# Kernel tuning notes

Hardware: AMD Instinct MI355X
Metric: run time of the kernel (lower is better)

The kernel has to match this reference:

```python
import jax, jax.numpy as jnp
import numpy as np
import math

D = 2048
NH = 16       # query heads
NKV = 4       # kv heads (GQA)
HD = 128
SOFTCLAMP = 50.0
ROPE_BASE = 10000.0
B = 4
SQ_VLM = 1024
SQ_ACT = 64
S_CACHE = 256


def _heads(x, n):
    # [B,S,n*HD] -> [B,n,S,HD]
    b, s, _ = x.shape
    return x.reshape(b, s, n, HD).transpose(0, 2, 1, 3)


def _rope_cos_sin(pos):
    # pos: [B,S] int -> cos,sin [B,1,S,HD]
    inv_freq = 1.0 / (ROPE_BASE ** (jnp.arange(0, HD, 2, dtype=jnp.float32) / HD))
    freqs = pos.astype(jnp.float32)[..., None] * inv_freq  # [B,S,HD/2]
    emb = jnp.concatenate([freqs, freqs], axis=-1)         # [B,S,HD]
    return jnp.cos(emb)[:, None], jnp.sin(emb)[:, None]


def _apply_rope(x, cos, sin):
    # x: [B,H,S,HD]
    x1, x2 = x[..., : HD // 2], x[..., HD // 2 :]
    rot = jnp.concatenate([-x2, x1], axis=-1)
    return x * cos + rot * sin


def setup_inputs() -> dict:
    key = jax.random.key(0)
    ks = jax.random.split(key, 16)
    sc = lambda d: 1.0 / math.sqrt(d)
    inp = {
        'attention_mask': jnp.zeros((B, 1, SQ_VLM + SQ_ACT, S_CACHE + SQ_VLM + SQ_ACT), jnp.float32),
        'pos_vlm': jnp.broadcast_to(jnp.arange(S_CACHE, S_CACHE + SQ_VLM, dtype=jnp.int32), (B, SQ_VLM)),
        'pos_action': jnp.broadcast_to(jnp.arange(S_CACHE + SQ_VLM, S_CACHE + SQ_VLM + SQ_ACT, dtype=jnp.int32), (B, SQ_ACT)),
        'h_vlm': jax.random.normal(ks[0], (B, SQ_VLM, D), jnp.float32),
        'h_action': jax.random.normal(ks[1], (B, SQ_ACT, D), jnp.float32),
        'k_cache': jax.random.normal(ks[2], (B, NKV, S_CACHE, HD), jnp.float32),
        'v_cache': jax.random.normal(ks[3], (B, NKV, S_CACHE, HD), jnp.float32),
        'Wq_vlm': jax.random.normal(ks[4], (D, NH * HD), jnp.float32) * sc(D),
        'Wk_vlm': jax.random.normal(ks[5], (D, NKV * HD), jnp.float32) * sc(D),
        'Wv_vlm': jax.random.normal(ks[6], (D, NKV * HD), jnp.float32) * sc(D),
        'Wq_act': jax.random.normal(ks[7], (D, NH * HD), jnp.float32) * sc(D),
        'Wk_act': jax.random.normal(ks[8], (D, NKV * HD), jnp.float32) * sc(D),
        'Wv_act': jax.random.normal(ks[9], (D, NKV * HD), jnp.float32) * sc(D),
        'Wo_act': jax.random.normal(ks[10], (NH * HD, D), jnp.float32) * sc(NH * HD),
    }
    return inp


def reference(attention_mask, pos_vlm, pos_action, h_vlm, h_action, k_cache, v_cache,
              Wq_vlm, Wk_vlm, Wv_vlm, Wq_act, Wk_act, Wv_act, Wo_act):
    group = NH // NKV

    def qkv(h, pos, Wq, Wk, Wv):
        q = _heads(h @ Wq, NH)
        k = _heads(h @ Wk, NKV)
        v = _heads(h @ Wv, NKV)
        cos, sin = _rope_cos_sin(pos)
        return _apply_rope(q, cos, sin), _apply_rope(k, cos, sin), v

    q_v, k_v, v_v = qkv(h_vlm, pos_vlm, Wq_vlm, Wk_vlm, Wv_vlm)
    q_a, k_a, v_a = qkv(h_action, pos_action, Wq_act, Wk_act, Wv_act)

    # repeat_kv (GQA) on every KV source, cached mixture first (append_non_active order)
    rep = lambda t: jnp.repeat(t, group, axis=1)  # [B,NKV,S,HD] -> [B,NH,S,HD]
    k = jnp.concatenate([rep(k_cache), rep(k_v), rep(k_a)], axis=2)
    v = jnp.concatenate([rep(v_cache), rep(v_v), rep(v_a)], axis=2)
    q = jnp.concatenate([q_v, q_a], axis=2)  # [B,NH,Sq,HD]

    scores = jnp.einsum('bhqd,bhkd->bhqk', q, k) / math.sqrt(HD)
    scores = jnp.tanh(scores / SOFTCLAMP) * SOFTCLAMP + attention_mask
    w = jax.nn.softmax(scores.astype(jnp.float32), axis=-1).astype(q.dtype)
    out = jnp.einsum('bhqk,bhkd->bhqd', w, v)
    out = out.transpose(0, 2, 1, 3).reshape(B, SQ_VLM + SQ_ACT, NH * HD)

    # split by q_lens; 'vlm' is in post_attn_skip_names -> no o_proj, dropped
    out_action = out[:, SQ_VLM:, :]
    return out_action @ Wo_act
```

## Files before the change

### kernel.cpp

```cpp
#include <hip/hip_runtime.h>
#include <cmath>

#define NH 16
#define NKV 4
#define HD 128
#define DMODEL 2048
#define BB 4
#define SQV 1024
#define SQA 64
#define SCACHE 256
#define STOT 1344
#define SQTOT 1088
#define NSPLIT 7

typedef unsigned short u16;
typedef __attribute__((ext_vector_type(8))) short short8;
typedef __attribute__((ext_vector_type(4))) float f32x4;

__device__ __forceinline__ float b2f(u16 u) {
    union { float f; unsigned int i; } x; x.i = ((unsigned int)u) << 16; return x.f;
}
__device__ __forceinline__ u16 f2b(float f) {
    unsigned int x = __float_as_uint(f);
    x = x + 0x7fffu + ((x >> 16) & 1u);
    return (u16)(x >> 16);
}

__global__ void k_prep(const float* __restrict__ mask,
                       const float* __restrict__ kc, const float* __restrict__ vc,
                       const float* __restrict__ hv, const float* __restrict__ ha,
                       float* __restrict__ cosT, float* __restrict__ sinT,
                       u16* __restrict__ maskS, u16* __restrict__ K_all, u16* __restrict__ V_all,
                       u16* __restrict__ hv16, u16* __restrict__ ha16) {
    int bx = blockIdx.x, tid = threadIdx.x;
    if (bx < 336) {
        int i = bx * 256 + tid;
        if (i < STOT * 64) {
            int p = i >> 6, j = i & 63;
            float inv = __expf(-(float)j * (9.210340371976184f / 64.0f));
            float ang = (float)p * inv;
            cosT[i] = cosf(ang);
            sinT[i] = sinf(ang);
        }
    } else if (bx < 1680) {
        int i = (bx - 336) * 256 + tid;
        int b = i / (SQA * STOT);
        int r = i % (SQA * STOT);
        size_t s = (size_t)b * SQTOT * STOT + (size_t)SQV * STOT + r;
        maskS[i] = f2b(mask[s]);
    } else if (bx < 1936) {
        int i = (bx - 1680) * 256 + tid;
        int e = i * 8;
        int bk = e / (SCACHE * HD);
        int off = e % (SCACHE * HD);
        size_t dst = (size_t)bk * STOT * HD + off;
        const float* fk = kc + e;
        const float* fv = vc + e;
        u16 tk[8], tv[8];
#pragma unroll
        for (int j = 0; j < 8; j++) { tk[j] = f2b(fk[j]); tv[j] = f2b(fv[j]); }
        *(short8*)(K_all + dst) = *(short8*)tk;
        *(short8*)(V_all + dst) = *(short8*)tv;
    } else if (bx < 6032) {
        int i = (bx - 1936) * 256 + tid;
        int e = i * 8;
        const float* f = hv + e;
        float4 a = *(const float4*)f, b = *(const float4*)(f + 4);
        u16 t[8] = {f2b(a.x), f2b(a.y), f2b(a.z), f2b(a.w),
                    f2b(b.x), f2b(b.y), f2b(b.z), f2b(b.w)};
        *(short8*)(hv16 + e) = *(short8*)t;
    } else {
        int i = (bx - 6032) * 256 + tid;
        int e = i * 8;
        const float* f = ha + e;
        float4 a = *(const float4*)f, b = *(const float4*)(f + 4);
        u16 t[8] = {f2b(a.x), f2b(a.y), f2b(a.z), f2b(a.w),
                    f2b(b.x), f2b(b.y), f2b(b.z), f2b(b.w)};
        *(short8*)(ha16 + e) = *(short8*)t;
    }
}

__device__ __forceinline__ void transpose_body(const float* in, u16* out, int N,
                                               int bx, int by) {
    __shared__ __align__(16) u16 t[64 * 66];
    int n0 = bx * 64, k0 = by * 64;
    int tid = threadIdx.x;
    int r = tid >> 3;
    int c8 = (tid & 7) * 8;
#pragma unroll
    for (int h = 0; h < 2; h++) {
        int k = r + h * 32;
        const float* f = in + (size_t)(k0 + k) * N + n0 + c8;
        float4 a = *(const float4*)f, b = *(const float4*)(f + 4);
        u16 vv[8] = {f2b(a.x), f2b(a.y), f2b(a.z), f2b(a.w),
                     f2b(b.x), f2b(b.y), f2b(b.z), f2b(b.w)};
#pragma unroll
        for (int j = 0; j < 8; j++) t[(c8 + j) * 66 + k] = vv[j];
    }
    __syncthreads();
#pragma unroll
    for (int h = 0; h < 2; h++) {
        int n = r + h * 32;
        short8 v;
#pragma unroll
        for (int j = 0; j < 8; j++) ((u16*)&v)[j] = t[n * 66 + c8 + j];
        *(short8*)(out + (size_t)(n0 + n) * 2048 + k0 + c8) = v;
    }
}

__global__ void k_transpose6(const float* w0, u16* o0, const float* w1, u16* o1,
                             const float* w2, u16* o2, const float* w3, u16* o3,
                             const float* w4, u16* o4, const float* w5, u16* o5) {
    int gx = blockIdx.x;
    if (gx < 256)        transpose_body(w0, o0, 512,  gx & 7,  gx >> 3);
    else if (gx < 512)   { int g = gx - 256;  transpose_body(w1, o1, 512,  g & 7,  g >> 3); }
    else if (gx < 768)   { int g = gx - 512;  transpose_body(w2, o2, 512,  g & 7,  g >> 3); }
    else if (gx < 1024)  { int g = gx - 768;  transpose_body(w3, o3, 512,  g & 7,  g >> 3); }
    else if (gx < 2048)  { int g = gx - 1024; transpose_body(w4, o4, 2048, g & 31, g >> 5); }
    else                 { int g = gx - 2048; transpose_body(w5, o5, 2048, g & 31, g >> 5); }
}

__global__ __launch_bounds__(256) void k_gemm_qkv(
    const u16* __restrict__ Avlm, const u16* __restrict__ Aact,
    const u16* __restrict__ WkvT, const u16* __restrict__ WvvT,
    const u16* __restrict__ WqaT, const u16* __restrict__ WkaT, const u16* __restrict__ WvaT,
    const int* __restrict__ pos_vlm, const int* __restrict__ pos_act,
    const float* __restrict__ cosT, const float* __restrict__ sinT,
    u16* __restrict__ Qbuf, u16* __restrict__ K_all, u16* __restrict__ V_all) {
    __shared__ __align__(16) u16 smem[64 * 72 + 128 * 72];
    u16* As = smem;
    u16* Bs = smem + 64 * 72;
    int tid = threadIdx.x;
    int w = tid >> 6, lane = tid & 63;
    int la = lane & 15, lg = lane >> 4;
    int wm = (w & 1) * 32;
    int c2 = w >> 1;
    int ntab[4] = {c2 * 2, c2 * 2 + 1, c2 * 2 + 4, c2 * 2 + 5};
    int vrow = tid >> 3, vcol = (tid & 7) * 8;

    const u16* A; const u16* Bt; int m0, n0;
    int path;
    int kv_or_head = 0;
    if (blockIdx.y < 8) {
        int by = blockIdx.y;
        m0 = blockIdx.x * 64;
        A = Avlm;
        path = (by < 4) ? 0 : 1;
        kv_or_head = by & 3;
        n0 = kv_or_head * 128;
        Bt = (path == 0) ? WkvT : WvvT;
    } else {
        int g = (blockIdx.y - 8) * 64 + blockIdx.x;
        if (g >= 96) return;
        m0 = (g & 3) * 64;
        int ny = g >> 2;
        A = Aact;
        if (ny < 16)      { path = 2; kv_or_head = ny;      Bt = WqaT; n0 = ny * 128; }
        else if (ny < 20) { path = 3; kv_or_head = ny - 16; Bt = WkaT; n0 = (ny - 16) * 128; }
        else              { path = 4; kv_or_head = ny - 20; Bt = WvaT; n0 = (ny - 20) * 128; }
    }

    f32x4 acc[2][4];
#pragma unroll
    for (int i = 0; i < 2; i++)
#pragma unroll
        for (int j = 0; j < 4; j++) acc[i][j] = (f32x4){0.f, 0.f, 0.f, 0.f};

    short8 pa[2], pb[4];
#pragma unroll
    for (int h = 0; h < 2; h++)
        pa[h] = *(const short8*)(A + (size_t)(m0 + vrow + h * 32) * DMODEL + vcol);
#pragma unroll
    for (int h = 0; h < 4; h++)
        pb[h] = *(const short8*)(Bt + (size_t)(n0 + vrow + h * 32) * DMODEL + vcol);

    for (int kb = 0; kb < DMODEL; kb += 64) {
#pragma unroll
        for (int h = 0; h < 2; h++)
            *(short8*)&As[(vrow + h * 32) * 72 + vcol] = pa[h];
#pragma unroll
        for (int h = 0; h < 4; h++)
            *(short8*)&Bs[(vrow + h * 32) * 72 + vcol] = pb[h];
        __syncthreads();
        int kn = (kb + 64 < DMODEL) ? kb + 64 : kb;
#pragma unroll
        for (int h = 0; h < 2; h++)
            pa[h] = *(const short8*)(A + (size_t)(m0 + vrow + h * 32) * DMODEL + kn + vcol);
#pragma unroll
        for (int h = 0; h < 4; h++)
            pb[h] = *(const short8*)(Bt + (size_t)(n0 + vrow + h * 32) * DMODEL + kn + vcol);
#pragma unroll
        for (int kk = 0; kk < 2; kk++) {
            short8 af[2], bf[4];
#pragma unroll
            for (int mt = 0; mt < 2; mt++) af[mt] = *(const short8*)&As[(wm + mt * 16 + la) * 72 + kk * 32 + lg * 8];
#pragma unroll
            for (int nt = 0; nt < 4; nt++) bf[nt] = *(const short8*)&Bs[(ntab[nt] * 16 + la) * 72 + kk * 32 + lg * 8];
#pragma unroll
            for (int mt = 0; mt < 2; mt++)
#pragma unroll
                for (int nt = 0; nt < 4; nt++)
                    acc[mt][nt] = __builtin_amdgcn_mfma_f32_16x16x32_bf16(af[mt], bf[nt], acc[mt][nt], 0, 0, 0);
        }
        __syncthreads();
    }

#pragma unroll
    for (int mt = 0; mt < 2; mt++) {
#pragma unroll
        for (int r = 0; r < 4; r++) {
            int gm = m0 + wm + mt * 16 + lg * 4 + r;
            if (path <= 1) {
                int b = gm >> 10, s = gm & 1023;
                size_t base = ((size_t)(b * NKV + kv_or_head) * STOT + SCACHE + s) * HD;
                if (path == 0) {
                    int pos = pos_vlm[gm];
#pragma unroll
                    for (int i = 0; i < 2; i++) {
                        int dlo = ntab[i] * 16 + la;
                        float x1 = acc[mt][i][r], x2 = acc[mt][i + 2][r];
                        float cs = cosT[pos * 64 + dlo], sn = sinT[pos * 64 + dlo];
                        K_all[base + dlo]      = f2b(x1 * cs - x2 * sn);
                        K_all[base + dlo + 64] = f2b(x2 * cs + x1 * sn);
                    }
                } else {
#pragma unroll
                    for (int i = 0; i < 4; i++) V_all[base + ntab[i] * 16 + la] = f2b(acc[mt][i][r]);
                }
            } else {
                int b = gm >> 6, s = gm & 63;
                if (path == 2) {
                    int pos = pos_act[gm];
                    size_t qb = ((size_t)(b * NH + kv_or_head) * SQA + s) * HD;
#pragma unroll
                    for (int i = 0; i < 2; i++) {
                        int dlo = ntab[i] * 16 + la;
                        float x1 = acc[mt][i][r], x2 = acc[mt][i + 2][r];
                        float cs = cosT[pos * 64 + dlo], sn = sinT[pos * 64 + dlo];
                        Qbuf[qb + dlo]      = f2b(x1 * cs - x2 * sn);
                        Qbuf[qb + dlo + 64] = f2b(x2 * cs + x1 * sn);
                    }
                } else if (path == 3) {
                    int pos = pos_act[gm];
                    size_t base = ((size_t)(b * NKV + kv_or_head) * STOT + SCACHE + SQV + s) * HD;
#pragma unroll
                    for (int i = 0; i < 2; i++) {
                        int dlo = ntab[i] * 16 + la;
                        float x1 = acc[mt][i][r], x2 = acc[mt][i + 2][r];
                        float cs = cosT[pos * 64 + dlo], sn = sinT[pos * 64 + dlo];
                        K_all[base + dlo]      = f2b(x1 * cs - x2 * sn);
                        K_all[base + dlo + 64] = f2b(x2 * cs + x1 * sn);
                    }
                } else {
                    size_t base = ((size_t)(b * NKV + kv_or_head) * STOT + SCACHE + SQV + s) * HD;
#pragma unroll
                    for (int i = 0; i < 4; i++) V_all[base + ntab[i] * 16 + la] = f2b(acc[mt][i][r]);
                }
            }
        }
    }
}

__global__ __launch_bounds__(256) void k_attn_split(
    const u16* __restrict__ Qbuf, const u16* __restrict__ K_all, const u16* __restrict__ V_all,
    const u16* __restrict__ maskS, u16* __restrict__ po, float* __restrict__ pml) {
    int h = blockIdx.x, b = blockIdx.y, p = blockIdx.z;
    int bh = b * NH + h;
    int kvh = h >> 2;
    const u16* Kb = K_all + (size_t)(b * NKV + kvh) * STOT * HD;
    const u16* Vb = V_all + (size_t)(b * NKV + kvh) * STOT * HD;
    const u16* Qb = Qbuf + (size_t)bh * SQA * HD;
    int tid = threadIdx.x, w = tid >> 6, lane = tid & 63;
    int la = lane & 15, lg = lane >> 4;
    __shared__ __align__(16) u16 Ks[64 * 136];
    __shared__ __align__(16) u16 Vs[64 * 130];
    __shared__ __align__(16) u16 Ps[4][16 * 72];
    short8 qf[4];
#pragma unroll
    for (int kk = 0; kk < 4; kk++)
        qf[kk] = *(const short8*)(Qb + (size_t)(w * 16 + la) * HD + kk * 32 + lg * 8);
    f32x4 o_acc[8];
#pragma unroll
    for (int nt = 0; nt < 8; nt++) o_acc[nt] = (f32x4){0.f, 0.f, 0.f, 0.f};
    float m_run[4], l_run[4];
#pragma unroll
    for (int r = 0; r < 4; r++) { m_run[r] = -3e38f; l_run[r] = 0.f; }
    int vr = tid >> 4;
    int vc = (tid & 15) * 8;
    const float scl = 0.08838834764831845f;
    for (int c = 0; c < 3; c++) {
        int g = p * 3 + c;
#pragma unroll
        for (int hh = 0; hh < 4; hh++) {
            int key = vr + hh * 16;
            *(short8*)&Ks[key * 136 + vc] = *(const short8*)(Kb + (size_t)(g * 64 + key) * HD + vc);
            short8 vv = *(const short8*)(Vb + (size_t)(g * 64 + key) * HD + vc);
            unsigned int* d32 = (unsigned int*)&Vs[key * 130 + vc];
#pragma unroll
            for (int q2 = 0; q2 < 4; q2++) d32[q2] = ((unsigned int*)&vv)[q2];
        }
        __syncthreads();
        f32x4 s_acc[4];
#pragma unroll
        for (int nt = 0; nt < 4; nt++) s_acc[nt] = (f32x4){0.f, 0.f, 0.f, 0.f};
#pragma unroll
        for (int kk = 0; kk < 4; kk++) {
#pragma unroll
            for (int nt = 0; nt < 4; nt++) {
                short8 kf = *(const short8*)&Ks[(nt * 16 + la) * 136 + kk * 32 + lg * 8];
                s_acc[nt] = __builtin_amdgcn_mfma_f32_16x16x32_bf16(qf[kk], kf, s_acc[nt], 0, 0, 0);
            }
        }
        float sc[4][4];
#pragma unroll
        for (int nt = 0; nt < 4; nt++) {
            int key = g * 64 + nt * 16 + la;
#pragma unroll
            for (int r = 0; r < 4; r++) {
                int sq = w * 16 + lg * 4 + r;
                float sv = s_acc[nt][r] * scl;
                sv = tanhf(sv * 0.02f) * 50.0f;
                sv += b2f(maskS[((size_t)(b * SQA + sq)) * STOT + key]);
                sc[nt][r] = sv;
            }
        }
#pragma unroll
        for (int r = 0; r < 4; r++) {
            float mx = fmaxf(fmaxf(sc[0][r], sc[1][r]), fmaxf(sc[2][r], sc[3][r]));
#pragma unroll
            for (int sh = 1; sh < 16; sh <<= 1) mx = fmaxf(mx, __shfl_xor(mx, sh, 64));
            float mn = fmaxf(m_run[r], mx);
            float alpha = __expf(m_run[r] - mn);
            m_run[r] = mn;
            float rowsum = 0.f;
#pragma unroll
            for (int nt = 0; nt < 4; nt++) {
                float pv = __expf(sc[nt][r] - mn);
                Ps[w][(lg * 4 + r) * 72 + nt * 16 + la] = f2b(pv);
                rowsum += pv;
            }
#pragma unroll
            for (int sh = 1; sh < 16; sh <<= 1) rowsum += __shfl_xor(rowsum, sh, 64);
            l_run[r] = l_run[r] * alpha + rowsum;
#pragma unroll
            for (int nt = 0; nt < 8; nt++) o_acc[nt][r] *= alpha;
        }
        __syncthreads();
#pragma unroll
        for (int kk = 0; kk < 2; kk++) {
            short8 pf = *(const short8*)&Ps[w][la * 72 + kk * 32 + lg * 8];
#pragma unroll
            for (int nt = 0; nt < 8; nt++) {
                short8 vf;
#pragma unroll
                for (int j = 0; j < 8; j++) ((u16*)&vf)[j] = Vs[(kk * 32 + lg * 8 + j) * 130 + nt * 16 + la];
                o_acc[nt] = __builtin_amdgcn_mfma_f32_16x16x32_bf16(pf, vf, o_acc[nt], 0, 0, 0);
            }
        }
        __syncthreads();
    }
#pragma unroll
    for (int nt = 0; nt < 8; nt++) {
#pragma unroll
        for (int r = 0; r < 4; r++) {
            int sq = w * 16 + lg * 4 + r;
            po[(((size_t)p * 64 + bh) * 64 + sq) * 128 + nt * 16 + la] = f2b(o_acc[nt][r]);
        }
    }
    if (la == 0) {
#pragma unroll
        for (int r = 0; r < 4; r++) {
            int sq = w * 16 + lg * 4 + r;
            size_t mlb = (((size_t)p * 64 + bh) * 64 + sq) * 2;
            pml[mlb] = m_run[r];
            pml[mlb + 1] = l_run[r];
        }
    }
}

__global__ __launch_bounds__(256) void k_attn_red(
    const u16* __restrict__ po, const float* __restrict__ pml, u16* __restrict__ AO) {
    int h = blockIdx.x, b = blockIdx.y;
    int bh = b * NH + h;
    __shared__ float wgt[NSPLIT][64];
    int tid = threadIdx.x;
    if (tid < 64) {
        int q = tid;
        float m[NSPLIT], l[NSPLIT], M = -3e38f;
#pragma unroll
        for (int p = 0; p < NSPLIT; p++) {
            size_t mlb = (((size_t)p * 64 + bh) * 64 + q) * 2;
            m[p] = pml[mlb]; l[p] = pml[mlb + 1];
            M = fmaxf(M, m[p]);
        }
        float L = 0.f;
#pragma unroll
        for (int p = 0; p < NSPLIT; p++) L += l[p] * __expf(m[p] - M);
        float inv = 1.0f / L;
#pragma unroll
        for (int p = 0; p < NSPLIT; p++) wgt[p][q] = __expf(m[p] - M) * inv;
    }
    __syncthreads();
    for (int e = tid; e < 64 * 128; e += 256) {
        int q = e >> 7, d = e & 127;
        float s = 0.f;
#pragma unroll
        for (int p = 0; p < NSPLIT; p++)
            s += b2f(po[(((size_t)p * 64 + bh) * 64 + q) * 128 + d]) * wgt[p][q];
        AO[((size_t)(b * SQA + q)) * 2048 + h * HD + d] = f2b(s);
    }
}

__global__ __launch_bounds__(256) void k_gemm_out(
    const u16* __restrict__ A, const u16* __restrict__ WoT, float* __restrict__ out) {
    __shared__ __align__(16) u16 As[64 * 72];
    __shared__ __align__(16) u16 Bs[64 * 72];
    int m0 = blockIdx.x * 64, n0 = blockIdx.y * 64;
    int tid = threadIdx.x;
    int w = tid >> 6, lane = tid & 63;
    int la = lane & 15, lg = lane >> 4;
    int wm = (w & 1) * 32, wn = (w >> 1) * 32;
    f32x4 acc[2][2];
#pragma unroll
    for (int i = 0; i < 2; i++)
#pragma unroll
        for (int j = 0; j < 2; j++) acc[i][j] = (f32x4){0.f, 0.f, 0.f, 0.f};
    int vrow = tid >> 3, vcol = (tid & 7) * 8;
    short8 pa[2], pb[2];
#pragma unroll
    for (int h = 0; h < 2; h++) {
        pa[h] = *(const short8*)(A   + (size_t)(m0 + vrow + h * 32) * DMODEL + vcol);
        pb[h] = *(const short8*)(WoT + (size_t)(n0 + vrow + h * 32) * DMODEL + vcol);
    }
    for (int kb = 0; kb < DMODEL; kb += 64) {
#pragma unroll
        for (int h = 0; h < 2; h++) {
            *(short8*)&As[(vrow + h * 32) * 72 + vcol] = pa[h];
            *(short8*)&Bs[(vrow + h * 32) * 72 + vcol] = pb[h];
        }
        __syncthreads();
        int kn = (kb + 64 < DMODEL) ? kb + 64 : kb;
#pragma unroll
        for (int h = 0; h < 2; h++) {
            pa[h] = *(const short8*)(A   + (size_t)(m0 + vrow + h * 32) * DMODEL + kn + vcol);
            pb[h] = *(const short8*)(WoT + (size_t)(n0 + vrow + h * 32) * DMODEL + kn + vcol);
        }
#pragma unroll
        for (int kk = 0; kk < 2; kk++) {
            short8 af[2], bf[2];
#pragma unroll
            for (int mt = 0; mt < 2; mt++) af[mt] = *(const short8*)&As[(wm + mt * 16 + la) * 72 + kk * 32 + lg * 8];
#pragma unroll
            for (int nt = 0; nt < 2; nt++) bf[nt] = *(const short8*)&Bs[(wn + nt * 16 + la) * 72 + kk * 32 + lg * 8];
#pragma unroll
            for (int mt = 0; mt < 2; mt++)
#pragma unroll
                for (int nt = 0; nt < 2; nt++)
                    acc[mt][nt] = __builtin_amdgcn_mfma_f32_16x16x32_bf16(af[mt], bf[nt], acc[mt][nt], 0, 0, 0);
        }
        __syncthreads();
    }
#pragma unroll
    for (int mt = 0; mt < 2; mt++) {
#pragma unroll
        for (int r = 0; r < 4; r++) {
            int gm = m0 + wm + mt * 16 + lg * 4 + r;
#pragma unroll
            for (int nt = 0; nt < 2; nt++)
                out[(size_t)gm * DMODEL + n0 + wn + nt * 16 + la] = acc[mt][nt][r];
        }
    }
}

extern "C" void kernel_launch(void* const* d_in, const int* in_sizes, int n_in,
                              void* d_out, int out_size, void* d_ws, size_t ws_size,
                              hipStream_t stream) {
    (void)in_sizes; (void)n_in; (void)out_size;
    const float* mask    = (const float*)d_in[0];
    const int*   pos_vlm = (const int*)d_in[1];
    const int*   pos_act = (const int*)d_in[2];
    const float* h_vlm   = (const float*)d_in[3];
    const float* h_act   = (const float*)d_in[4];
    const float* k_cache = (const float*)d_in[5];
    const float* v_cache = (const float*)d_in[6];
    const float* Wk_vlm  = (const float*)d_in[8];
    const float* Wv_vlm  = (const float*)d_in[9];
    const float* Wq_act  = (const float*)d_in[10];
    const float* Wk_act  = (const float*)d_in[11];
    const float* Wv_act  = (const float*)d_in[12];
    const float* Wo_act  = (const float*)d_in[13];

    const size_t NEED = 65273856;
    if (ws_size < NEED) return;
    char* ws = (char*)d_ws;
    float* cosT  = (float*)(ws + 0);
    float* sinT  = (float*)(ws + 344064);
    u16* K_all   = (u16*)(ws + 688128);
    u16* V_all   = (u16*)(ws + 6193152);
    u16* Qbuf    = (u16*)(ws + 11698176);
    u16* AO      = (u16*)(ws + 12746752);
    u16* WkvT    = (u16*)(ws + 13795328);
    u16* WvvT    = (u16*)(ws + 15892480);
    u16* WqaT    = (u16*)(ws + 17989632);
    u16* WkaT    = (u16*)(ws + 26378240);
    u16* WvaT    = (u16*)(ws + 28475392);
    u16* WoT     = (u16*)(ws + 30572544);
    u16* po      = (u16*)(ws + 38961152);
    float* pml   = (float*)(ws + 46301184);
    u16* maskS   = (u16*)(ws + 46759936);
    u16* hv16    = (u16*)(ws + 47448064);
    u16* ha16    = (u16*)(ws + 64225280);

    hipLaunchKernelGGL(k_prep, dim3(6288), dim3(256), 0, stream,
                       mask, k_cache, v_cache, h_vlm, h_act,
                       cosT, sinT, maskS, K_all, V_all, hv16, ha16);
    hipLaunchKernelGGL(k_transpose6, dim3(3072), dim3(256), 0, stream,
                       Wk_vlm, WkvT, Wv_vlm, WvvT, Wk_act, WkaT, Wv_act, WvaT,
                       Wq_act, WqaT, Wo_act, WoT);
    hipLaunchKernelGGL(k_gemm_qkv, dim3(64, 10), dim3(256), 0, stream,
                       hv16, ha16, WkvT, WvvT, WqaT, WkaT, WvaT,
                       pos_vlm, pos_act, cosT, sinT, Qbuf, K_all, V_all);
    hipLaunchKernelGGL(k_attn_split, dim3(16, 4, NSPLIT), dim3(256), 0, stream,
                       Qbuf, K_all, V_all, maskS, po, pml);
    hipLaunchKernelGGL(k_attn_red, dim3(16, 4), dim3(256), 0, stream, po, pml, AO);
    hipLaunchKernelGGL(k_gemm_out, dim3(4, 32), dim3(256), 0, stream, AO, WoT, (float*)d_out);
}
```

Baseline: 253.4 us.

## Merge transpose into prep, use async LDS double-buffering in GEMMs, fast tanh

Folds the weight transpose/convert kernel into the prep kernel, removing one launch. Both bf16 GEMMs switch from register-staged copies to direct global-to-LDS loads with a double buffer and XOR swizzle, so the next K-tile's loads overlap the current tile's MFMAs. The softclamp tanh in attention is replaced with an exp-based formula. The changes trade extra LDS use and hand-placed waitcnt/barrier ordering for overlap, and the fast tanh carries a small accuracy risk.

Measured after the change: 239.1 us. -5.6%, faster.

```diff
diff --git a/kernel.cpp b/kernel.cpp
--- a/kernel.cpp
+++ b/kernel.cpp
@@ -26,13 +26,62 @@
     return (u16)(x >> 16);
 }
 
+__device__ __forceinline__ void gload16(const void* g, void* l) {
+    __builtin_amdgcn_global_load_lds((const __attribute__((address_space(1))) void*)g,
+                                     (__attribute__((address_space(3))) void*)l, 16, 0, 0);
+}
+
+__device__ __forceinline__ void transpose_body(const float* in, u16* out, int N,
+                                               int bx, int by) {
+    __shared__ __align__(16) u16 t[64 * 66];
+    int n0 = bx * 64, k0 = by * 64;
+    int tid = threadIdx.x;
+    int r = tid >> 3;
+    int c8 = (tid & 7) * 8;
+#pragma unroll
+    for (int h = 0; h < 2; h++) {
+        int k = r + h * 32;
+        const float* f = in + (size_t)(k0 + k) * N + n0 + c8;
+        float4 a = *(const float4*)f, b = *(const float4*)(f + 4);
+        u16 vv[8] = {f2b(a.x), f2b(a.y), f2b(a.z), f2b(a.w),
+                     f2b(b.x), f2b(b.y), f2b(b.z), f2b(b.w)};
+#pragma unroll
+        for (int j = 0; j < 8; j++) t[(c8 + j) * 66 + k] = vv[j];
+    }
+    __syncthreads();
+#pragma unroll
+    for (int h = 0; h < 2; h++) {
+        int n = r + h * 32;
+        short8 v;
+#pragma unroll
+        for (int j = 0; j < 8; j++) ((u16*)&v)[j] = t[n * 66 + c8 + j];
+        *(short8*)(out + (size_t)(n0 + n) * 2048 + k0 + c8) = v;
+    }
+}
+
 __global__ void k_prep(const float* __restrict__ mask,
                        const float* __restrict__ kc, const float* __restrict__ vc,
                        const float* __restrict__ hv, const float* __restrict__ ha,
+                       const float* __restrict__ w0, u16* __restrict__ o0,
+                       const float* __restrict__ w1, u16* __restrict__ o1,
+                       const float* __restrict__ w2, u16* __restrict__ o2,
+                       const float* __restrict__ w3, u16* __restrict__ o3,
+                       const float* __restrict__ w4, u16* __restrict__ o4,
+                       const float* __restrict__ w5, u16* __restrict__ o5,
                        float* __restrict__ cosT, float* __restrict__ sinT,
                        u16* __restrict__ maskS, u16* __restrict__ K_all, u16* __restrict__ V_all,
                        u16* __restrict__ hv16, u16* __restrict__ ha16) {
-    int bx = blockIdx.x, tid = threadIdx.x;
+    int gx = blockIdx.x, tid = threadIdx.x;
+    if (gx < 3072) {
+        if (gx < 256)        transpose_body(w0, o0, 512,  gx & 7,  gx >> 3);
+        else if (gx < 512)   { int g = gx - 256;  transpose_body(w1, o1, 512,  g & 7,  g >> 3); }
+        else if (gx < 768)   { int g = gx - 512;  transpose_body(w2, o2, 512,  g & 7,  g >> 3); }
+        else if (gx < 1024)  { int g = gx - 768;  transpose_body(w3, o3, 512,  g & 7,  g >> 3); }
+        else if (gx < 2048)  { int g = gx - 1024; transpose_body(w4, o4, 2048, g & 31, g >> 5); }
+        else                 { int g = gx - 2048; transpose_body(w5, o5, 2048, g & 31, g >> 5); }
+        return;
+    }
+    int bx = gx - 3072;
     if (bx < 336) {
         int i = bx * 256 + tid;
         if (i < STOT * 64) {
@@ -80,46 +129,6 @@
     }
 }
 
-__device__ __forceinline__ void transpose_body(const float* in, u16* out, int N,
-                                               int bx, int by) {
-    __shared__ __align__(16) u16 t[64 * 66];
-    int n0 = bx * 64, k0 = by * 64;
-    int tid = threadIdx.x;
-    int r = tid >> 3;
-    int c8 = (tid & 7) * 8;
-#pragma unroll
-    for (int h = 0; h < 2; h++) {
-        int k = r + h * 32;
-        const float* f = in + (size_t)(k0 + k) * N + n0 + c8;
-        float4 a = *(const float4*)f, b = *(const float4*)(f + 4);
-        u16 vv[8] = {f2b(a.x), f2b(a.y), f2b(a.z), f2b(a.w),
-                     f2b(b.x), f2b(b.y), f2b(b.z), f2b(b.w)};
-#pragma unroll
-        for (int j = 0; j < 8; j++) t[(c8 + j) * 66 + k] = vv[j];
-    }
-    __syncthreads();
-#pragma unroll
-    for (int h = 0; h < 2; h++) {
-        int n = r + h * 32;
-        short8 v;
-#pragma unroll
-        for (int j = 0; j < 8; j++) ((u16*)&v)[j] = t[n * 66 + c8 + j];
-        *(short8*)(out + (size_t)(n0 + n) * 2048 + k0 + c8) = v;
-    }
-}
-
-__global__ void k_transpose6(const float* w0, u16* o0, const float* w1, u16* o1,
-                             const float* w2, u16* o2, const float* w3, u16* o3,
-                             const float* w4, u16* o4, const float* w5, u16* o5) {
-    int gx = blockIdx.x;
-    if (gx < 256)        transpose_body(w0, o0, 512,  gx & 7,  gx >> 3);
-    else if (gx < 512)   { int g = gx - 256;  transpose_body(w1, o1, 512,  g & 7,  g >> 3); }
-    else if (gx < 768)   { int g = gx - 512;  transpose_body(w2, o2, 512,  g & 7,  g >> 3); }
-    else if (gx < 1024)  { int g = gx - 768;  transpose_body(w3, o3, 512,  g & 7,  g >> 3); }
-    else if (gx < 2048)  { int g = gx - 1024; transpose_body(w4, o4, 2048, g & 31, g >> 5); }
-    else                 { int g = gx - 2048; transpose_body(w5, o5, 2048, g & 31, g >> 5); }
-}
-
 __global__ __launch_bounds__(256) void k_gemm_qkv(
     const u16* __restrict__ Avlm, const u16* __restrict__ Aact,
     const u16* __restrict__ WkvT, const u16* __restrict__ WvvT,
@@ -127,16 +136,13 @@
     const int* __restrict__ pos_vlm, const int* __restrict__ pos_act,
     const float* __restrict__ cosT, const float* __restrict__ sinT,
     u16* __restrict__ Qbuf, u16* __restrict__ K_all, u16* __restrict__ V_all) {
-    __shared__ __align__(16) u16 smem[64 * 72 + 128 * 72];
-    u16* As = smem;
-    u16* Bs = smem + 64 * 72;
+    __shared__ __align__(16) u16 smem[2 * 12288];
     int tid = threadIdx.x;
     int w = tid >> 6, lane = tid & 63;
     int la = lane & 15, lg = lane >> 4;
     int wm = (w & 1) * 32;
     int c2 = w >> 1;
     int ntab[4] = {c2 * 2, c2 * 2 + 1, c2 * 2 + 4, c2 * 2 + 5};
-    int vrow = tid >> 3, vcol = (tid & 7) * 8;
 
     const u16* A; const u16* Bt; int m0, n0;
     int path;
@@ -166,44 +172,56 @@
 #pragma unroll
         for (int j = 0; j < 4; j++) acc[i][j] = (f32x4){0.f, 0.f, 0.f, 0.f};
 
-    short8 pa[2], pb[4];
-#pragma unroll
-    for (int h = 0; h < 2; h++)
-        pa[h] = *(const short8*)(A + (size_t)(m0 + vrow + h * 32) * DMODEL + vcol);
-#pragma unroll
-    for (int h = 0; h < 4; h++)
-        pb[h] = *(const short8*)(Bt + (size_t)(n0 + vrow + h * 32) * DMODEL + vcol);
-
+    int srow = tid >> 3;
+    int scsrc = (((tid & 7) * 16) ^ ((srow & 7) << 4)) >> 1;
+
+#define STAGE_QKV(CB, KB) do {                                                        \
+        u16* Ab_ = smem + (CB) * 12288;                                               \
+        u16* Bb_ = Ab_ + 4096;                                                        \
+        _Pragma("unroll")                                                             \
+        for (int h = 0; h < 2; h++)                                                   \
+            gload16(A + (size_t)(m0 + srow + h * 32) * DMODEL + (KB) + scsrc,         \
+                    Ab_ + h * 2048 + w * 512);                                        \
+        _Pragma("unroll")                                                             \
+        for (int h = 0; h < 4; h++)                                                   \
+            gload16(Bt + (size_t)(n0 + srow + h * 32) * DMODEL + (KB) + scsrc,        \
+                    Bb_ + h * 2048 + w * 512);                                        \
+    } while (0)
+
+    STAGE_QKV(0, 0);
+    int cur = 0;
+    int sw = (la & 7) << 3;
     for (int kb = 0; kb < DMODEL; kb += 64) {
-#pragma unroll
-        for (int h = 0; h < 2; h++)
-            *(short8*)&As[(vrow + h * 32) * 72 + vcol] = pa[h];
-#pragma unroll
-        for (int h = 0; h < 4; h++)
-            *(short8*)&Bs[(vrow + h * 32) * 72 + vcol] = pb[h];
-        __syncthreads();
-        int kn = (kb + 64 < DMODEL) ? kb + 64 : kb;
-#pragma unroll
-        for (int h = 0; h < 2; h++)
-            pa[h] = *(const short8*)(A + (size_t)(m0 + vrow + h * 32) * DMODEL + kn + vcol);
-#pragma unroll
-        for (int h = 0; h < 4; h++)
-            pb[h] = *(const short8*)(Bt + (size_t)(n0 + vrow + h * 32) * DMODEL + kn + vcol);
+        if (kb + 64 < DMODEL) {
+            STAGE_QKV(cur ^ 1, kb + 64);
+            asm volatile("s_waitcnt vmcnt(6)" ::: "memory");
+        } else {
+            asm volatile("s_waitcnt vmcnt(0)" ::: "memory");
+        }
+        __builtin_amdgcn_s_barrier();
+        asm volatile("" ::: "memory");
+        const u16* Ac = smem + cur * 12288;
+        const u16* Bc = Ac + 4096;
 #pragma unroll
         for (int kk = 0; kk < 2; kk++) {
             short8 af[2], bf[4];
-#pragma unroll
-            for (int mt = 0; mt < 2; mt++) af[mt] = *(const short8*)&As[(wm + mt * 16 + la) * 72 + kk * 32 + lg * 8];
-#pragma unroll
-            for (int nt = 0; nt < 4; nt++) bf[nt] = *(const short8*)&Bs[(ntab[nt] * 16 + la) * 72 + kk * 32 + lg * 8];
+            int cc = (kk * 32 + lg * 8) ^ sw;
+#pragma unroll
+            for (int mt = 0; mt < 2; mt++)
+                af[mt] = *(const short8*)&Ac[(wm + mt * 16 + la) * 64 + cc];
+#pragma unroll
+            for (int nt = 0; nt < 4; nt++)
+                bf[nt] = *(const short8*)&Bc[(ntab[nt] * 16 + la) * 64 + cc];
 #pragma unroll
             for (int mt = 0; mt < 2; mt++)
 #pragma unroll
                 for (int nt = 0; nt < 4; nt++)
                     acc[mt][nt] = __builtin_amdgcn_mfma_f32_16x16x32_bf16(af[mt], bf[nt], acc[mt][nt], 0, 0, 0);
         }
-        __syncthreads();
-    }
+        __builtin_amdgcn_s_barrier();
+        cur ^= 1;
+    }
+#undef STAGE_QKV
 
 #pragma unroll
     for (int mt = 0; mt < 2; mt++) {
@@ -319,7 +337,10 @@
             for (int r = 0; r < 4; r++) {
                 int sq = w * 16 + lg * 4 + r;
                 float sv = s_acc[nt][r] * scl;
-                sv = tanhf(sv * 0.02f) * 50.0f;
+                float x = sv * 0.02f;
+                float t = __expf(-2.0f * fabsf(x));
+                float th = __fdividef(1.0f - t, 1.0f + t);
+                sv = copysignf(th, x) * 50.0f;
                 sv += b2f(maskS[((size_t)(b * SQA + sq)) * STOT + key]);
                 sc[nt][r] = sv;
             }
@@ -413,8 +434,7 @@
 
 __global__ __launch_bounds__(256) void k_gemm_out(
     const u16* __restrict__ A, const u16* __restrict__ WoT, float* __restrict__ out) {
-    __shared__ __align__(16) u16 As[64 * 72];
-    __shared__ __align__(16) u16 Bs[64 * 72];
+    __shared__ __align__(16) u16 smem[2 * 8192];
     int m0 = blockIdx.x * 64, n0 = blockIdx.y * 64;
     int tid = threadIdx.x;
     int w = tid >> 6, lane = tid & 63;
@@ -425,41 +445,56 @@
     for (int i = 0; i < 2; i++)
 #pragma unroll
         for (int j = 0; j < 2; j++) acc[i][j] = (f32x4){0.f, 0.f, 0.f, 0.f};
-    int vrow = tid >> 3, vcol = (tid & 7) * 8;
-    short8 pa[2], pb[2];
-#pragma unroll
-    for (int h = 0; h < 2; h++) {
-        pa[h] = *(const short8*)(A   + (size_t)(m0 + vrow + h * 32) * DMODEL + vcol);
-        pb[h] = *(const short8*)(WoT + (size_t)(n0 + vrow + h * 32) * DMODEL + vcol);
-    }
+
+    int srow = tid >> 3;
+    int scsrc = (((tid & 7) * 16) ^ ((srow & 7) << 4)) >> 1;
+
+#define STAGE_OUT(CB, KB) do {                                                        \
+        u16* Ab_ = smem + (CB) * 8192;                                                \
+        u16* Bb_ = Ab_ + 4096;                                                        \
+        _Pragma("unroll")                                                             \
+        for (int h = 0; h < 2; h++)                                                   \
+            gload16(A + (size_t)(m0 + srow + h * 32) * DMODEL + (KB) + scsrc,         \
+                    Ab_ + h * 2048 + w * 512);                                        \
+        _Pragma("unroll")                                                             \
+        for (int h = 0; h < 2; h++)                                                   \
+            gload16(WoT + (size_t)(n0 + srow + h * 32) * DMODEL + (KB) + scsrc,       \
+                    Bb_ + h * 2048 + w * 512);                                        \
+    } while (0)
+
+    STAGE_OUT(0, 0);
+    int cur = 0;
+    int sw = (la & 7) << 3;
     for (int kb = 0; kb < DMODEL; kb += 64) {
-#pragma unroll
-        for (int h = 0; h < 2; h++) {
-            *(short8*)&As[(vrow + h * 32) * 72 + vcol] = pa[h];
-            *(short8*)&Bs[(vrow + h * 32) * 72 + vcol] = pb[h];
-        }
-        __syncthreads();
-        int kn = (kb + 64 < DMODEL) ? kb + 64 : kb;
-#pragma unroll
-        for (int h = 0; h < 2; h++) {
-            pa[h] = *(const short8*)(A   + (size_t)(m0 + vrow + h * 32) * DMODEL + kn + vcol);
-            pb[h] = *(const short8*)(WoT + (size_t)(n0 + vrow + h * 32) * DMODEL + kn + vcol);
-        }
+        if (kb + 64 < DMODEL) {
+            STAGE_OUT(cur ^ 1, kb + 64);
+            asm volatile("s_waitcnt vmcnt(4)" ::: "memory");
+        } else {
+            asm volatile("s_waitcnt vmcnt(0)" ::: "memory");
+        }
+        __builtin_amdgcn_s_barrier();
+        asm volatile("" ::: "memory");
+        const u16* Ac = smem + cur * 8192;
+        const u16* Bc = Ac + 4096;
 #pragma unroll
         for (int kk = 0; kk < 2; kk++) {
             short8 af[2], bf[2];
-#pragma unroll
-            for (int mt = 0; mt < 2; mt++) af[mt] = *(const short8*)&As[(wm + mt * 16 + la) * 72 + kk * 32 + lg * 8];
-#pragma unroll
-            for (int nt = 0; nt < 2; nt++) bf[nt] = *(const short8*)&Bs[(wn + nt * 16 + la) * 72 + kk * 32 + lg * 8];
+            int cc = (kk * 32 + lg * 8) ^ sw;
+#pragma unroll
+            for (int mt = 0; mt < 2; mt++) af[mt] = *(const short8*)&Ac[(wm + mt * 16 + la) * 64 + cc];
+#pragma unroll
+            for (int nt = 0; nt < 2; nt++) bf[nt] = *(const short8*)&Bc[(wn + nt * 16 + la) * 64 + cc];
 #pragma unroll
             for (int mt = 0; mt < 2; mt++)
 #pragma unroll
                 for (int nt = 0; nt < 2; nt++)
                     acc[mt][nt] = __builtin_amdgcn_mfma_f32_16x16x32_bf16(af[mt], bf[nt], acc[mt][nt], 0, 0, 0);
         }
-        __syncthreads();
-    }
+        __builtin_amdgcn_s_barrier();
+        cur ^= 1;
+    }
+#undef STAGE_OUT
+
 #pragma unroll
     for (int mt = 0; mt < 2; mt++) {
 #pragma unroll
@@ -511,12 +546,11 @@
     u16* hv16    = (u16*)(ws + 47448064);
     u16* ha16    = (u16*)(ws + 64225280);
 
-    hipLaunchKernelGGL(k_prep, dim3(6288), dim3(256), 0, stream,
+    hipLaunchKernelGGL(k_prep, dim3(9360), dim3(256), 0, stream,
                        mask, k_cache, v_cache, h_vlm, h_act,
+                       Wk_vlm, WkvT, Wv_vlm, WvvT, Wk_act, WkaT, Wv_act, WvaT,
+                       Wq_act, WqaT, Wo_act, WoT,
                        cosT, sinT, maskS, K_all, V_all, hv16, ha16);
-    hipLaunchKernelGGL(k_transpose6, dim3(3072), dim3(256), 0, stream,
-                       Wk_vlm, WkvT, Wv_vlm, WvvT, Wk_act, WkaT, Wv_act, WvaT,
-                       Wq_act, WqaT, Wo_act, WoT);
     hipLaunchKernelGGL(k_gemm_qkv, dim3(64, 10), dim3(256), 0, stream,
                        hv16, ha16, WkvT, WvvT, WqaT, WkaT, WvaT,
                        pos_vlm, pos_act, cosT, sinT, Qbuf, K_all, V_all);
```
